# Performance work log

Measured on AMD Instinct MI355X. Metric: run time of the kernel, lower is better.

Reference implementation:

```python
import jax, jax.numpy as jnp
import numpy as np

DIM = 1024
HEADS = 16
HEAD_DIM = DIM // HEADS
SCALE = HEAD_DIM ** -0.5


def setup_inputs() -> dict:
    key = jax.random.key(0)
    k1, k2, k3, k4 = jax.random.split(key, 4)
    x = jax.random.normal(k1, (2, 2048, DIM), dtype=jnp.float32)
    s = DIM ** -0.5
    qkv_w = jax.random.normal(k2, (3 * DIM, DIM), dtype=jnp.float32) * s
    proj_w = jax.random.normal(k3, (DIM, DIM), dtype=jnp.float32) * s
    proj_b = jax.random.normal(k4, (DIM,), dtype=jnp.float32) * 0.01
    return {"x": x, "qkv_w": qkv_w, "proj_w": proj_w, "proj_b": proj_b}


def reference(x, qkv_w, proj_w, proj_b):
    B, N, C = x.shape
    # qkv: Linear(dim, 3*dim) with torch convention y = x @ W^T
    qkv = jnp.einsum('bnc,dc->bnd', x, qkv_w)
    qkv = qkv.reshape(B, N, 3, HEADS, HEAD_DIM).transpose(2, 0, 3, 1, 4)
    q, k, v = qkv[0], qkv[1], qkv[2]           # [B, H, N, Dh]
    attn = jnp.einsum('bhnd,bhmd->bhnm', q, k) * SCALE
    attn = jax.nn.softmax(attn, axis=-1)
    out = jnp.einsum('bhnm,bhmd->bhnd', attn, v)  # [B, H, N, Dh]
    out = out.transpose(0, 2, 1, 3).reshape(B, N, C)
    out = jnp.einsum('bnc,dc->bnd', out, proj_w) + proj_b
    return out
```

## Files before the change

kernel.cpp:

```cpp
#include <hip/hip_runtime.h>
#include <cmath>


namespace {
constexpr int kDim   = 1024;
constexpr int kHeads = 16;
constexpr int kHd    = 64;
constexpr int kB     = 2;
constexpr int kN     = 2048;
constexpr int kM     = kB * kN;
constexpr float kScale  = 0.125f;
constexpr float kQScale = 0.125f * 1.44269504088896f;
constexpr int kP = 72;
}

typedef __attribute__((ext_vector_type(8))) short bf16x8;
typedef __attribute__((ext_vector_type(4))) float f32x4;

#if __has_builtin(__builtin_amdgcn_exp2f)
#define EXP2(x) __builtin_amdgcn_exp2f(x)
#else
#define EXP2(x) __expf((x) * 0.6931471805599453f)
#endif

__device__ inline unsigned short f2bf(float x) {
  union { float f; unsigned u; } un; un.f = x;
  unsigned r = un.u + 0x7fffu + ((un.u >> 16) & 1u);
  return (unsigned short)(r >> 16);
}
__device__ inline short tbf(float x) {
  union { float f; unsigned u; } un; un.f = x;
  return (short)(un.u >> 16);
}
__device__ inline unsigned pack2bf(float x, float y) {
  return (unsigned)f2bf(x) | ((unsigned)f2bf(y) << 16);
}
__device__ inline void gl_lds16(const short* g, short* l) {
  __builtin_amdgcn_global_load_lds(
      (const __attribute__((address_space(1))) unsigned*)g,
      (__attribute__((address_space(3))) unsigned*)l, 16, 0, 0);
}

__global__ __launch_bounds__(256) void cvt3_kernel(
    const float* __restrict__ a, short* __restrict__ da, int n0,
    const float* __restrict__ b, short* __restrict__ db, int n1,
    const float* __restrict__ c, short* __restrict__ dc) {
  int blk = blockIdx.x;
  const float* src; short* dst;
  if (blk < n0) { src = a; dst = da; }
  else if (blk < n0 + n1) { src = b; dst = db; blk -= n0; }
  else { src = c; dst = dc; blk -= n0 + n1; }
  const int i = (blk * 256 + threadIdx.x) * 8;
  float4 u = *(const float4*)&src[i];
  float4 v = *(const float4*)&src[i + 4];
  bf16x8 o = {(short)f2bf(u.x), (short)f2bf(u.y), (short)f2bf(u.z), (short)f2bf(u.w),
              (short)f2bf(v.x), (short)f2bf(v.y), (short)f2bf(v.z), (short)f2bf(v.w)};
  *(bf16x8*)&dst[i] = o;
}

__global__ __launch_bounds__(256, 2) void mm_qkv_kernel(
    const short* __restrict__ A16, const short* __restrict__ W16,
    short* __restrict__ q16, short* __restrict__ k16, short* __restrict__ vT16) {
  __shared__ short smem[2 * 128 * 64];
  short* As = smem;
  short* Bs = smem + 128 * 64;
  const int tid  = threadIdx.x;
  const int w    = tid >> 6;
  const int lane = tid & 63;
  const int quad = lane >> 4;
  const int k15  = lane & 15;
  const int m0   = blockIdx.x * 128;
  const int seg  = blockIdx.y >> 3;
  const int nt0  = (blockIdx.y & 7) << 7;
  const int wrow0 = seg * 1024 + nt0;
  const int wm = (w >> 1) * 64;
  const int wn = (w & 1) * 64;
  const int lrow   = lane >> 3;
  const int lchunk = (lane & 7) ^ lrow;

  f32x4 acc[4][4];
#pragma unroll
  for (int i = 0; i < 4; ++i)
#pragma unroll
    for (int j = 0; j < 4; ++j) acc[i][j] = (f32x4){0.f, 0.f, 0.f, 0.f};

  for (int kt = 0; kt < 1024; kt += 64) {
    __syncthreads();
#pragma unroll
    for (int p = 0; p < 4; ++p) {
      const int r0 = p * 32 + w * 8;
      gl_lds16(&A16[(long)(m0 + r0 + lrow) * 1024 + kt + lchunk * 8], &As[r0 * 64]);
      gl_lds16(&W16[(long)(wrow0 + r0 + lrow) * 1024 + kt + lchunk * 8], &Bs[r0 * 64]);
    }
    __syncthreads();
#pragma unroll
    for (int ks = 0; ks < 2; ++ks) {
      bf16x8 af[4], bf[4];
#pragma unroll
      for (int t = 0; t < 4; ++t) {
        const int Ra = wm + t * 16 + k15;
        af[t] = *(const bf16x8*)&As[Ra * 64 + (((ks << 2) + quad) ^ (Ra & 7)) * 8];
        const int Rb = wn + t * 16 + k15;
        bf[t] = *(const bf16x8*)&Bs[Rb * 64 + (((ks << 2) + quad) ^ (Rb & 7)) * 8];
      }
#pragma unroll
      for (int mt = 0; mt < 4; ++mt)
#pragma unroll
        for (int nt = 0; nt < 4; ++nt)
          acc[mt][nt] = __builtin_amdgcn_mfma_f32_16x16x32_bf16(
              af[mt], bf[nt], acc[mt][nt], 0, 0, 0);
    }
  }

  if (seg < 2) {
    short* dst = (seg == 0) ? q16 : k16;
    const float sc = (seg == 0) ? kQScale : 1.0f;
#pragma unroll
    for (int nt = 0; nt < 4; ++nt) {
      const int dl = nt0 + wn + nt * 16 + k15;
      const int h  = dl >> 6;
      const int dh = dl & 63;
#pragma unroll
      for (int mt = 0; mt < 4; ++mt) {
#pragma unroll
        for (int r = 0; r < 4; ++r) {
          const int ml = m0 + wm + mt * 16 + quad * 4 + r;
          const int b  = ml >> 11;
          const int n  = ml & 2047;
          dst[(((long)(b * kHeads + h) * kN) + n) * kHd + dh] =
              (short)f2bf(acc[mt][nt][r] * sc);
        }
      }
    }
  } else {
    __syncthreads();
    short* Tw = smem + w * 16 * kP;
#pragma unroll
    for (int nt = 0; nt < 4; ++nt) {
#pragma unroll
      for (int mt = 0; mt < 4; ++mt) {
        uint2 pk;
        pk.x = pack2bf(acc[mt][nt][0], acc[mt][nt][1]);
        pk.y = pack2bf(acc[mt][nt][2], acc[mt][nt][3]);
        *(uint2*)&Tw[k15 * kP + mt * 16 + quad * 4] = pk;
      }
#pragma unroll
      for (int i = 0; i < 2; ++i) {
        const int idx  = i * 64 + lane;
        const int trow = idx >> 3;
        const int tch  = idx & 7;
        bf16x8 row = *(const bf16x8*)&Tw[trow * kP + tch * 8];
        const int vcol = nt0 + wn + nt * 16 + trow;
        const int h  = vcol >> 6;
        const int dh = vcol & 63;
        const int m  = m0 + wm + tch * 8;
        const int b  = m >> 11;
        const int n  = m & 2047;
        *(bf16x8*)&vT16[(((long)(b * kHeads + h) * kHd) + dh) * kN + n] = row;
      }
    }
  }
}

__global__ __launch_bounds__(256, 2) void mm_proj_kernel(
    const short* __restrict__ A16, const short* __restrict__ B16,
    const float* __restrict__ bias, float* __restrict__ out) {
  __shared__ short As[128 * 64];
  __shared__ short Bs[128 * 64];
  const int tid  = threadIdx.x;
  const int w    = tid >> 6;
  const int lane = tid & 63;
  const int quad = lane >> 4;
  const int k15  = lane & 15;
  const int m0 = blockIdx.x * 128;
  const int n0 = blockIdx.y * 128;
  const int wm = (w >> 1) * 64;
  const int wn = (w & 1) * 64;
  const int lrow   = lane >> 3;
  const int lchunk = (lane & 7) ^ lrow;

  f32x4 acc[4][4];
#pragma unroll
  for (int i = 0; i < 4; ++i)
#pragma unroll
    for (int j = 0; j < 4; ++j) acc[i][j] = (f32x4){0.f, 0.f, 0.f, 0.f};

  for (int kt = 0; kt < 1024; kt += 64) {
    __syncthreads();
#pragma unroll
    for (int p = 0; p < 4; ++p) {
      const int r0 = p * 32 + w * 8;
      gl_lds16(&A16[(long)(m0 + r0 + lrow) * 1024 + kt + lchunk * 8], &As[r0 * 64]);
      gl_lds16(&B16[(long)(n0 + r0 + lrow) * 1024 + kt + lchunk * 8], &Bs[r0 * 64]);
    }
    __syncthreads();
#pragma unroll
    for (int ks = 0; ks < 2; ++ks) {
      bf16x8 af[4], bf[4];
#pragma unroll
      for (int t = 0; t < 4; ++t) {
        const int Ra = wm + t * 16 + k15;
        af[t] = *(const bf16x8*)&As[Ra * 64 + (((ks << 2) + quad) ^ (Ra & 7)) * 8];
        const int Rb = wn + t * 16 + k15;
        bf[t] = *(const bf16x8*)&Bs[Rb * 64 + (((ks << 2) + quad) ^ (Rb & 7)) * 8];
      }
#pragma unroll
      for (int mt = 0; mt < 4; ++mt)
#pragma unroll
        for (int nt = 0; nt < 4; ++nt)
          acc[mt][nt] = __builtin_amdgcn_mfma_f32_16x16x32_bf16(
              af[mt], bf[nt], acc[mt][nt], 0, 0, 0);
    }
  }

#pragma unroll
  for (int nt = 0; nt < 4; ++nt) {
    const int d = n0 + wn + nt * 16 + k15;
    const float bb = bias[d];
#pragma unroll
    for (int mt = 0; mt < 4; ++mt) {
#pragma unroll
      for (int r = 0; r < 4; ++r) {
        const int m = m0 + wm + mt * 16 + quad * 4 + r;
        out[(long)m * 1024 + d] = acc[mt][nt][r] + bb;
      }
    }
  }
}

__global__ __launch_bounds__(256, 2) void attn_kernel(
    const short* __restrict__ q16, const short* __restrict__ k16,
    const short* __restrict__ vT16, short* __restrict__ ao16) {
  __shared__ short Ks[128 * 64];
  __shared__ short Vs[64 * 128];
  __shared__ short Ps[4 * 2 * 16 * kP];

  const int tid  = threadIdx.x;
  const int w    = tid >> 6;
  const int lane = tid & 63;
  const int quad = lane >> 4;
  const int k15  = lane & 15;
  const int lrow  = lane >> 3;
  const int lch8  = lane & 7;
  const int lrow4 = lane >> 4;
  const int lch16 = lane & 15;
  const int bufIdx = blockIdx.z * kHeads + blockIdx.y;
  const long base  = (long)bufIdx * kN * kHd;

  bf16x8 qf[2][2];
#pragma unroll
  for (int qt = 0; qt < 2; ++qt) {
    const long qr = base + (long)(blockIdx.x * 128 + w * 32 + qt * 16 + k15) * kHd;
#pragma unroll
    for (int ks = 0; ks < 2; ++ks)
      qf[qt][ks] = *(const bf16x8*)&q16[qr + ks * 32 + quad * 8];
  }

  const short oneb = (short)0x3F80;
  bf16x8 onesf;
#pragma unroll
  for (int j = 0; j < 8; ++j) onesf[j] = (k15 == 0) ? oneb : (short)0;

  f32x4 accO[2][4];
#pragma unroll
  for (int qt = 0; qt < 2; ++qt)
#pragma unroll
    for (int d = 0; d < 4; ++d) accO[qt][d] = (f32x4){0.f, 0.f, 0.f, 0.f};
  f32x4 accL[2] = {{0.f,0.f,0.f,0.f},{0.f,0.f,0.f,0.f}};

  for (int kt = 0; kt < kN / 128; ++kt) {
    __syncthreads();
    {
      const short* kg = k16 + base + (long)kt * 128 * kHd;
      const short* vg = vT16 + base + kt * 128;
#pragma unroll
      for (int c = 0; c < 4; ++c) {
        const int r0 = w * 32 + c * 8;
        gl_lds16(kg + (long)(r0 + lrow) * kHd + (lch8 ^ ((r0 + lrow) & 7)) * 8,
                 &Ks[r0 * 64]);
      }
#pragma unroll
      for (int c = 0; c < 4; ++c) {
        const int r0v = w * 16 + c * 4;
        gl_lds16(vg + (long)(r0v + lrow4) * kN + (lch16 ^ ((r0v + lrow4) & 15)) * 8,
                 &Vs[r0v * 128]);
      }
    }
    __syncthreads();

#pragma unroll
    for (int h2 = 0; h2 < 2; ++h2) {
      bf16x8 kb[4][2];
#pragma unroll
      for (int t = 0; t < 4; ++t) {
        const int row = h2 * 64 + t * 16 + k15;
#pragma unroll
        for (int ks = 0; ks < 2; ++ks)
          kb[t][ks] = *(const bf16x8*)&Ks[row * 64 + (((ks << 2) + quad) ^ (row & 7)) * 8];
      }
      bf16x8 vb[2][4];
#pragma unroll
      for (int kc = 0; kc < 2; ++kc)
#pragma unroll
        for (int d = 0; d < 4; ++d) {
          const int vrow = d * 16 + k15;
          const int ch = (h2 * 8 + kc * 4 + quad) ^ (vrow & 15);
          vb[kc][d] = *(const bf16x8*)&Vs[vrow * 128 + ch * 8];
        }

#pragma unroll
      for (int qt = 0; qt < 2; ++qt) {
        f32x4 sc[4];
#pragma unroll
        for (int t = 0; t < 4; ++t) {
          f32x4 z = {0.f, 0.f, 0.f, 0.f};
          z = __builtin_amdgcn_mfma_f32_16x16x32_bf16(qf[qt][0], kb[t][0], z, 0, 0, 0);
          z = __builtin_amdgcn_mfma_f32_16x16x32_bf16(qf[qt][1], kb[t][1], z, 0, 0, 0);
          sc[t] = z;
        }
        short* pw = Ps + (w * 2 + qt) * 16 * kP;
#pragma unroll
        for (int t = 0; t < 4; ++t)
#pragma unroll
          for (int r = 0; r < 4; ++r)
            pw[(quad * 4 + r) * kP + t * 16 + k15] = tbf(EXP2(sc[t][r]));
#pragma unroll
        for (int kc = 0; kc < 2; ++kc) {
          bf16x8 pf = *(const bf16x8*)&pw[k15 * kP + kc * 32 + quad * 8];
#pragma unroll
          for (int d = 0; d < 4; ++d)
            accO[qt][d] = __builtin_amdgcn_mfma_f32_16x16x32_bf16(
                pf, vb[kc][d], accO[qt][d], 0, 0, 0);
          accL[qt] = __builtin_amdgcn_mfma_f32_16x16x32_bf16(
              pf, onesf, accL[qt], 0, 0, 0);
        }
      }
    }
  }

#pragma unroll
  for (int qt = 0; qt < 2; ++qt) {
#pragma unroll
    for (int r = 0; r < 4; ++r) {
      const float s  = __shfl(accL[qt][r], (lane & 48));
      const float in = 1.f / s;
      const int gq = blockIdx.x * 128 + w * 32 + qt * 16 + quad * 4 + r;
      short* drow = ao16 + ((long)(blockIdx.z * kN + gq)) * kDim + blockIdx.y * kHd;
#pragma unroll
      for (int d = 0; d < 4; ++d)
        drow[d * 16 + k15] = (short)f2bf(accO[qt][d][r] * in);
    }
  }
}

__global__ __launch_bounds__(256, 2) void r3_qkv_kernel(
    const float* __restrict__ X, const float* __restrict__ W,
    short* __restrict__ q16, short* __restrict__ k16, short* __restrict__ v16) {
  __shared__ short As[128 * kP];
  __shared__ short Ws[128 * kP];
  const int tid  = threadIdx.x;
  const int w    = tid >> 6;
  const int lane = tid & 63;
  const int quad = lane >> 4;
  const int k15  = lane & 15;
  const int m0 = blockIdx.x * 128;
  const int n0 = blockIdx.y * 128;
  const int wm = (w >> 1) * 64;
  const int wn = (w & 1) * 64;

  f32x4 acc[4][4];
#pragma unroll
  for (int i = 0; i < 4; ++i)
#pragma unroll
    for (int j = 0; j < 4; ++j) acc[i][j] = (f32x4){0.f, 0.f, 0.f, 0.f};

  for (int kt = 0; kt < kDim; kt += 64) {
    __syncthreads();
#pragma unroll
    for (int p = 0; p < 8; ++p) {
      const int idx = p * 256 + tid;
      const int row = idx >> 4;
      const int c4  = (idx & 15) << 2;
      float4 av = *(const float4*)&X[(long)(m0 + row) * kDim + kt + c4];
      uint2 ap = {pack2bf(av.x, av.y), pack2bf(av.z, av.w)};
      *(uint2*)&As[row * kP + c4] = ap;
      float4 wv = *(const float4*)&W[(long)(n0 + row) * kDim + kt + c4];
      uint2 wp = {pack2bf(wv.x, wv.y), pack2bf(wv.z, wv.w)};
      *(uint2*)&Ws[row * kP + c4] = wp;
    }
    __syncthreads();
#pragma unroll
    for (int ks = 0; ks < 2; ++ks) {
      bf16x8 af[4], bf[4];
#pragma unroll
      for (int t = 0; t < 4; ++t) {
        af[t] = *(const bf16x8*)&As[(wm + t * 16 + k15) * kP + ks * 32 + quad * 8];
        bf[t] = *(const bf16x8*)&Ws[(wn + t * 16 + k15) * kP + ks * 32 + quad * 8];
      }
#pragma unroll
      for (int mt = 0; mt < 4; ++mt)
#pragma unroll
        for (int nt = 0; nt < 4; ++nt)
          acc[mt][nt] = __builtin_amdgcn_mfma_f32_16x16x32_bf16(
              af[mt], bf[nt], acc[mt][nt], 0, 0, 0);
    }
  }

  const int t_sel = n0 >> 10;
  short* dst = (t_sel == 0) ? q16 : (t_sel == 1) ? k16 : v16;
  const float scl = (t_sel == 0) ? kScale : 1.0f;
#pragma unroll
  for (int nt = 0; nt < 4; ++nt) {
    const int d  = n0 + wn + nt * 16 + k15;
    const int h  = (d >> 6) & 15;
    const int dh = d & 63;
#pragma unroll
    for (int mt = 0; mt < 4; ++mt) {
#pragma unroll
      for (int r = 0; r < 4; ++r) {
        const int m = m0 + wm + mt * 16 + quad * 4 + r;
        dst[((long)h * kN + m) * kHd + dh] = (short)f2bf(acc[mt][nt][r] * scl);
      }
    }
  }
}

__global__ __launch_bounds__(256, 4) void attn_v1_kernel(
    const short* __restrict__ q16, const short* __restrict__ k16,
    const short* __restrict__ v16, short* __restrict__ ao16, int bpar) {
  __shared__ short Ks[64 * kP];
  __shared__ short Vs[64 * kP];
  __shared__ short Ps[4 * 16 * kP];
  const int tid  = threadIdx.x;
  const int w    = tid >> 6;
  const int lane = tid & 63;
  const int quad = lane >> 4;
  const int k15  = lane & 15;
  const long base = (long)blockIdx.y * kN * kHd;
  const int qrow = blockIdx.x * 64 + w * 16 + k15;
  const short* qp = q16 + base + (long)qrow * kHd + quad * 8;
  bf16x8 qf0 = *(const bf16x8*)(qp);
  bf16x8 qf1 = *(const bf16x8*)(qp + 32);

  f32x4 accO[4] = {{0.f,0.f,0.f,0.f},{0.f,0.f,0.f,0.f},
                   {0.f,0.f,0.f,0.f},{0.f,0.f,0.f,0.f}};
  float lsum[4] = {0.f, 0.f, 0.f, 0.f};

  for (int kt = 0; kt < kN / 64; ++kt) {
    __syncthreads();
    {
      const short* kg = k16 + base + (long)kt * 64 * kHd;
      const short* vg = v16 + base + (long)kt * 64 * kHd;
#pragma unroll
      for (int p = 0; p < 2; ++p) {
        const int idx = p * 256 + tid;
        const int key = idx >> 3;
        const int c8  = (idx & 7) << 3;
        *(bf16x8*)&Ks[key * kP + c8] = *(const bf16x8*)&kg[key * kHd + c8];
        bf16x8 vv = *(const bf16x8*)&vg[key * kHd + c8];
#pragma unroll
        for (int j = 0; j < 8; ++j) Vs[(c8 + j) * kP + key] = vv[j];
      }
    }
    __syncthreads();

    f32x4 sc[4];
#pragma unroll
    for (int t = 0; t < 4; ++t) {
      bf16x8 kb0 = *(const bf16x8*)&Ks[(t * 16 + k15) * kP + quad * 8];
      bf16x8 kb1 = *(const bf16x8*)&Ks[(t * 16 + k15) * kP + 32 + quad * 8];
      f32x4 z = {0.f, 0.f, 0.f, 0.f};
      z = __builtin_amdgcn_mfma_f32_16x16x32_bf16(qf0, kb0, z, 0, 0, 0);
      z = __builtin_amdgcn_mfma_f32_16x16x32_bf16(qf1, kb1, z, 0, 0, 0);
      sc[t] = z;
    }
    short* pw = &Ps[w * (16 * kP)];
#pragma unroll
    for (int t = 0; t < 4; ++t) {
#pragma unroll
      for (int r = 0; r < 4; ++r) {
        const float p = __expf(sc[t][r]);
        lsum[r] += p;
        pw[(quad * 4 + r) * kP + t * 16 + k15] = (short)f2bf(p);
      }
    }
    bf16x8 pf0 = *(const bf16x8*)&pw[k15 * kP + quad * 8];
    bf16x8 pf1 = *(const bf16x8*)&pw[k15 * kP + 32 + quad * 8];
#pragma unroll
    for (int t = 0; t < 4; ++t) {
      bf16x8 vb0 = *(const bf16x8*)&Vs[(t * 16 + k15) * kP + quad * 8];
      bf16x8 vb1 = *(const bf16x8*)&Vs[(t * 16 + k15) * kP + 32 + quad * 8];
      accO[t] = __builtin_amdgcn_mfma_f32_16x16x32_bf16(pf0, vb0, accO[t], 0, 0, 0);
      accO[t] = __builtin_amdgcn_mfma_f32_16x16x32_bf16(pf1, vb1, accO[t], 0, 0, 0);
    }
  }

#pragma unroll
  for (int r = 0; r < 4; ++r) {
    float s = lsum[r];
    s += __shfl_xor(s, 1);
    s += __shfl_xor(s, 2);
    s += __shfl_xor(s, 4);
    s += __shfl_xor(s, 8);
    lsum[r] = 1.f / s;
  }
#pragma unroll
  for (int r = 0; r < 4; ++r) {
    const int gq = blockIdx.x * 64 + w * 16 + quad * 4 + r;
    short* drow = ao16 + ((long)(bpar * kN + gq)) * kDim + blockIdx.y * kHd;
#pragma unroll
    for (int t = 0; t < 4; ++t)
      drow[t * 16 + k15] = (short)f2bf(accO[t][r] * lsum[r]);
  }
}

__global__ __launch_bounds__(256, 2) void r3_proj_kernel(
    const short* __restrict__ A16, const float* __restrict__ W,
    const float* __restrict__ bias, float* __restrict__ out) {
  __shared__ short As[128 * kP];
  __shared__ short Ws[128 * kP];
  const int tid  = threadIdx.x;
  const int w    = tid >> 6;
  const int lane = tid & 63;
  const int quad = lane >> 4;
  const int k15  = lane & 15;
  const int m0 = blockIdx.x * 128;
  const int n0 = blockIdx.y * 128;
  const int wm = (w >> 1) * 64;
  const int wn = (w & 1) * 64;

  f32x4 acc[4][4];
#pragma unroll
  for (int i = 0; i < 4; ++i)
#pragma unroll
    for (int j = 0; j < 4; ++j) acc[i][j] = (f32x4){0.f, 0.f, 0.f, 0.f};

  for (int kt = 0; kt < kDim; kt += 64) {
    __syncthreads();
#pragma unroll
    for (int p = 0; p < 4; ++p) {
      const int idx = p * 256 + tid;
      const int row = idx >> 3;
      const int c8  = (idx & 7) << 3;
      *(bf16x8*)&As[row * kP + c8] =
          *(const bf16x8*)&A16[(long)(m0 + row) * kDim + kt + c8];
    }
#pragma unroll
    for (int p = 0; p < 8; ++p) {
      const int idx = p * 256 + tid;
      const int row = idx >> 4;
      const int c4  = (idx & 15) << 2;
      float4 wv = *(const float4*)&W[(long)(n0 + row) * kDim + kt + c4];
      uint2 wp = {pack2bf(wv.x, wv.y), pack2bf(wv.z, wv.w)};
      *(uint2*)&Ws[row * kP + c4] = wp;
    }
    __syncthreads();
#pragma unroll
    for (int ks = 0; ks < 2; ++ks) {
      bf16x8 af[4], bf[4];
#pragma unroll
      for (int t = 0; t < 4; ++t) {
        af[t] = *(const bf16x8*)&As[(wm + t * 16 + k15) * kP + ks * 32 + quad * 8];
        bf[t] = *(const bf16x8*)&Ws[(wn + t * 16 + k15) * kP + ks * 32 + quad * 8];
      }
#pragma unroll
      for (int mt = 0; mt < 4; ++mt)
#pragma unroll
        for (int nt = 0; nt < 4; ++nt)
          acc[mt][nt] = __builtin_amdgcn_mfma_f32_16x16x32_bf16(
              af[mt], bf[nt], acc[mt][nt], 0, 0, 0);
    }
  }

#pragma unroll
  for (int nt = 0; nt < 4; ++nt) {
    const int d = n0 + wn + nt * 16 + k15;
    const float bb = bias[d];
#pragma unroll
    for (int mt = 0; mt < 4; ++mt) {
#pragma unroll
      for (int r = 0; r < 4; ++r) {
        const int m = m0 + wm + mt * 16 + quad * 4 + r;
        out[(long)m * kDim + d] = acc[mt][nt][r] + bb;
      }
    }
  }
}

extern "C" void kernel_launch(void* const* d_in, const int* in_sizes, int n_in,
                              void* d_out, int out_size, void* d_ws, size_t ws_size,
                              hipStream_t stream) {
  const float* x      = (const float*)d_in[0];
  const float* qkv_w  = (const float*)d_in[1];
  const float* proj_w = (const float*)d_in[2];
  const float* proj_b = (const float*)d_in[3];
  float* out = (float*)d_out;

  short* ws = (short*)d_ws;
  const size_t MiS = 1048576;

  if (ws_size >= 41943040ull) {
    short* X16  = ws;
    short* W16  = ws + 4 * MiS;
    short* PW16 = ws + 7 * MiS;
    short* q16  = ws + 8 * MiS;
    short* k16  = ws + 12 * MiS;
    short* vT16 = ws + 16 * MiS;
    short* ao16 = X16;

    cvt3_kernel<<<4096, 256, 0, stream>>>(x, X16, 2048, qkv_w, W16, 1536,
                                          proj_w, PW16);
    mm_qkv_kernel<<<dim3(32, 24), 256, 0, stream>>>(X16, W16, q16, k16, vT16);
    attn_kernel<<<dim3(16, 16, 2), 256, 0, stream>>>(q16, k16, vT16, ao16);
    mm_proj_kernel<<<dim3(32, 8), 256, 0, stream>>>(ao16, PW16, proj_b, out);
    return;
  }

  {
    short* q16  = ws;
    short* k16  = ws + 2 * MiS;
    short* v16  = ws + 4 * MiS;
    short* ao16 = ws + 6 * MiS;
    for (int b = 0; b < kB; ++b) {
      r3_qkv_kernel<<<dim3(16, 24), 256, 0, stream>>>(
          x + (size_t)b * kN * kDim, qkv_w, q16, k16, v16);
      attn_v1_kernel<<<dim3(32, 16), 256, 0, stream>>>(q16, k16, v16, ao16, b);
    }
    r3_proj_kernel<<<dim3(32, 8), 256, 0, stream>>>(ao16, proj_w, proj_b, out);
  }
}
```

Baseline: 177.9 us.

## Double-buffer K/V tiles in attention kernel with 64-key stages

Splits the attention K/V staging from one 128-key tile per iteration into double-buffered 64-key tiles in LDS. The next tile's async global-to-LDS load is issued right after the barrier so it overlaps with the MFMA work on the current tile, and one of the two barriers per iteration is dropped. The trade-off is twice as many loop iterations and barriers overall, and the V swizzle changes to an 8-chunk pattern that may affect bank conflicts.

```diff
diff --git a/kernel.cpp b/kernel.cpp
--- a/kernel.cpp
+++ b/kernel.cpp
@@ -231,8 +231,8 @@
 __global__ __launch_bounds__(256, 2) void attn_kernel(
     const short* __restrict__ q16, const short* __restrict__ k16,
     const short* __restrict__ vT16, short* __restrict__ ao16) {
-  __shared__ short Ks[128 * 64];
-  __shared__ short Vs[64 * 128];
+  __shared__ short Ks[2][64 * 64];
+  __shared__ short Vs[2][64 * 64];
   __shared__ short Ps[4 * 2 * 16 * kP];
 
   const int tid  = threadIdx.x;
@@ -240,12 +240,12 @@
   const int lane = tid & 63;
   const int quad = lane >> 4;
   const int k15  = lane & 15;
-  const int lrow  = lane >> 3;
+  const int lrow8 = lane >> 3;
   const int lch8  = lane & 7;
-  const int lrow4 = lane >> 4;
-  const int lch16 = lane & 15;
   const int bufIdx = blockIdx.z * kHeads + blockIdx.y;
   const long base  = (long)bufIdx * kN * kHd;
+  const short* kgb = k16 + base;
+  const short* vgb = vT16 + base;
 
   bf16x8 qf[2][2];
 #pragma unroll
@@ -268,75 +268,75 @@
     for (int d = 0; d < 4; ++d) accO[qt][d] = (f32x4){0.f, 0.f, 0.f, 0.f};
   f32x4 accL[2] = {{0.f,0.f,0.f,0.f},{0.f,0.f,0.f,0.f}};
 
-  for (int kt = 0; kt < kN / 128; ++kt) {
-    __syncthreads();
-    {
-      const short* kg = k16 + base + (long)kt * 128 * kHd;
-      const short* vg = vT16 + base + kt * 128;
-#pragma unroll
-      for (int c = 0; c < 4; ++c) {
-        const int r0 = w * 32 + c * 8;
-        gl_lds16(kg + (long)(r0 + lrow) * kHd + (lch8 ^ ((r0 + lrow) & 7)) * 8,
-                 &Ks[r0 * 64]);
-      }
-#pragma unroll
-      for (int c = 0; c < 4; ++c) {
-        const int r0v = w * 16 + c * 4;
-        gl_lds16(vg + (long)(r0v + lrow4) * kN + (lch16 ^ ((r0v + lrow4) & 15)) * 8,
-                 &Vs[r0v * 128]);
-      }
-    }
-    __syncthreads();
-
-#pragma unroll
-    for (int h2 = 0; h2 < 2; ++h2) {
-      bf16x8 kb[4][2];
+  const int srow = w * 16;
+#define STAGE(kt, b)                                                          \
+  {                                                                           \
+    const short* kg = kgb + (long)(kt) * 64 * kHd;                            \
+    const short* vg = vgb + (kt) * 64;                                        \
+    _Pragma("unroll")                                                         \
+    for (int c = 0; c < 2; ++c) {                                             \
+      const int r0 = srow + c * 8;                                            \
+      const int rr = r0 + lrow8;                                              \
+      gl_lds16(kg + (long)rr * kHd + (lch8 ^ (rr & 7)) * 8,                   \
+               &Ks[b][r0 * 64]);                                              \
+      gl_lds16(vg + (long)rr * kN + (lch8 ^ (rr & 7)) * 8,                    \
+               &Vs[b][r0 * 64]);                                              \
+    }                                                                         \
+  }
+
+  STAGE(0, 0);
+
+  for (int kt = 0; kt < kN / 64; ++kt) {
+    const int buf = kt & 1;
+    __syncthreads();
+    if (kt + 1 < kN / 64) STAGE(kt + 1, buf ^ 1);
+
+    bf16x8 kb[4][2];
+#pragma unroll
+    for (int t = 0; t < 4; ++t) {
+      const int row = t * 16 + k15;
+#pragma unroll
+      for (int ks = 0; ks < 2; ++ks)
+        kb[t][ks] = *(const bf16x8*)&Ks[buf][row * 64 + (((ks << 2) + quad) ^ (row & 7)) * 8];
+    }
+    bf16x8 vb[2][4];
+#pragma unroll
+    for (int kc = 0; kc < 2; ++kc)
+#pragma unroll
+      for (int d = 0; d < 4; ++d) {
+        const int vrow = d * 16 + k15;
+        vb[kc][d] = *(const bf16x8*)&Vs[buf][vrow * 64 + (((kc << 2) + quad) ^ (vrow & 7)) * 8];
+      }
+
+#pragma unroll
+    for (int qt = 0; qt < 2; ++qt) {
+      f32x4 sc[4];
 #pragma unroll
       for (int t = 0; t < 4; ++t) {
-        const int row = h2 * 64 + t * 16 + k15;
-#pragma unroll
-        for (int ks = 0; ks < 2; ++ks)
-          kb[t][ks] = *(const bf16x8*)&Ks[row * 64 + (((ks << 2) + quad) ^ (row & 7)) * 8];
-      }
-      bf16x8 vb[2][4];
-#pragma unroll
-      for (int kc = 0; kc < 2; ++kc)
-#pragma unroll
-        for (int d = 0; d < 4; ++d) {
-          const int vrow = d * 16 + k15;
-          const int ch = (h2 * 8 + kc * 4 + quad) ^ (vrow & 15);
-          vb[kc][d] = *(const bf16x8*)&Vs[vrow * 128 + ch * 8];
-        }
-
-#pragma unroll
-      for (int qt = 0; qt < 2; ++qt) {
-        f32x4 sc[4];
-#pragma unroll
-        for (int t = 0; t < 4; ++t) {
-          f32x4 z = {0.f, 0.f, 0.f, 0.f};
-          z = __builtin_amdgcn_mfma_f32_16x16x32_bf16(qf[qt][0], kb[t][0], z, 0, 0, 0);
-          z = __builtin_amdgcn_mfma_f32_16x16x32_bf16(qf[qt][1], kb[t][1], z, 0, 0, 0);
-          sc[t] = z;
-        }
-        short* pw = Ps + (w * 2 + qt) * 16 * kP;
-#pragma unroll
-        for (int t = 0; t < 4; ++t)
-#pragma unroll
-          for (int r = 0; r < 4; ++r)
-            pw[(quad * 4 + r) * kP + t * 16 + k15] = tbf(EXP2(sc[t][r]));
-#pragma unroll
-        for (int kc = 0; kc < 2; ++kc) {
-          bf16x8 pf = *(const bf16x8*)&pw[k15 * kP + kc * 32 + quad * 8];
-#pragma unroll
-          for (int d = 0; d < 4; ++d)
-            accO[qt][d] = __builtin_amdgcn_mfma_f32_16x16x32_bf16(
-                pf, vb[kc][d], accO[qt][d], 0, 0, 0);
-          accL[qt] = __builtin_amdgcn_mfma_f32_16x16x32_bf16(
-              pf, onesf, accL[qt], 0, 0, 0);
-        }
-      }
-    }
-  }
+        f32x4 z = {0.f, 0.f, 0.f, 0.f};
+        z = __builtin_amdgcn_mfma_f32_16x16x32_bf16(qf[qt][0], kb[t][0], z, 0, 0, 0);
+        z = __builtin_amdgcn_mfma_f32_16x16x32_bf16(qf[qt][1], kb[t][1], z, 0, 0, 0);
+        sc[t] = z;
+      }
+      short* pw = Ps + (w * 2 + qt) * 16 * kP;
+#pragma unroll
+      for (int t = 0; t < 4; ++t)
+#pragma unroll
+        for (int r = 0; r < 4; ++r)
+          pw[(quad * 4 + r) * kP + t * 16 + k15] = tbf(EXP2(sc[t][r]));
+#pragma unroll
+      for (int kc = 0; kc < 2; ++kc) {
+        bf16x8 pf = *(const bf16x8*)&pw[k15 * kP + kc * 32 + quad * 8];
+#pragma unroll
+        for (int d = 0; d < 4; ++d)
+          accO[qt][d] = __builtin_amdgcn_mfma_f32_16x16x32_bf16(
+              pf, vb[kc][d], accO[qt][d], 0, 0, 0);
+        accL[qt] = __builtin_amdgcn_mfma_f32_16x16x32_bf16(
+            pf, onesf, accL[qt], 0, 0, 0);
+      }
+    }
+  }
+#undef STAGE
 
 #pragma unroll
   for (int qt = 0; qt < 2; ++qt) {
```

After: 185.4 us. 4.2% more time.
